# Kernel optimization log

Hardware: AMD Instinct MI355X
Metric: run time of the kernel (lower is better)

Reference implementation:

```python
import jax, jax.numpy as jnp
import numpy as np

C = 128          # channel_size
H = 2            # num_head
HD = C // H      # per-head dim = 64
SCALE = C ** 0.5 # note: module scales by sqrt(channel_size), not sqrt(head_dim)


def setup_inputs() -> dict:
    key = jax.random.key(0)
    k_x, k_w, k_b = jax.random.split(key, 3)
    x = jax.random.normal(k_x, (8, 64, 256, C), dtype=jnp.float32)
    # nn.Linear(C, 3C): weight [3C, C], bias [3C]; y = x @ W.T + b
    bound = 1.0 / np.sqrt(C)
    W_qkv = jax.random.uniform(k_w, (3 * C, C), dtype=jnp.float32, minval=-bound, maxval=bound)
    b_qkv = jax.random.uniform(k_b, (3 * C,), dtype=jnp.float32, minval=-bound, maxval=bound)
    return {"x": x, "W_qkv": W_qkv, "b_qkv": b_qkv}


def reference(x, W_qkv, b_qkv):
    b, l, g, _ = x.shape
    qkv = jnp.einsum('blgc,dc->blgd', x, W_qkv) + b_qkv        # [b,l,g,3C]
    # rearrange 'b l g (d h c) -> d b l h g c'
    qkv = qkv.reshape(b, l, g, 3, H, HD)
    qkv = jnp.transpose(qkv, (3, 0, 1, 4, 2, 5))               # [3,b,l,h,g,c]
    q, k, v = qkv[0], qkv[1], qkv[2]
    score = jnp.einsum('blhgc,blhkc->blhgk', q, k) / SCALE      # [b,l,h,g,g]
    score = jax.nn.softmax(score, axis=-1)
    out = jnp.einsum('blhgk,blhkc->blhgc', score, v)            # [b,l,h,g,c]
    # rearrange 'b l h g c -> b l g (h c)'
    out = jnp.transpose(out, (0, 1, 3, 2, 4)).reshape(b, l, g, H * HD)
    return out
```

## Files before the change

### kernel.cpp

```cpp
#include <hip/hip_runtime.h>
#include <hip/hip_bf16.h>


typedef __bf16 bf16x8 __attribute__((ext_vector_type(8)));
typedef float  f32x4  __attribute__((ext_vector_type(4)));

#define MFMA16(a, b, c) __builtin_amdgcn_mfma_f32_16x16x32_bf16((a), (b), (c), 0, 0, 0)

namespace dmsa {

constexpr int G  = 256;
constexpr int C  = 128;
constexpr int HD = 64;
constexpr float QSCALE = 1.4426950408889634f * 0.08838834764831845f;

__device__ __forceinline__ unsigned pack2(float a, float b) {
    union { __hip_bfloat162 h; unsigned u; } c;
    c.h = __float22bfloat162_rn(make_float2(a, b));
    return c.u;
}
__device__ __forceinline__ uint2 pack4(float a, float b, float c, float d) {
    uint2 r; r.x = pack2(a, b); r.y = pack2(c, d); return r;
}
__device__ __forceinline__ uint4 pack8(const float* p) {
    uint4 r;
    r.x = pack2(p[0], p[1]); r.y = pack2(p[2], p[3]);
    r.z = pack2(p[4], p[5]); r.w = pack2(p[6], p[7]);
    return r;
}
__device__ __forceinline__ bf16x8 lds8(const ushort* p) { return *(const bf16x8*)p; }
__device__ __forceinline__ bf16x8 ldg8(const ushort* p) { return *(const bf16x8*)p; }

__global__ void convw(const float* __restrict__ W, ushort* __restrict__ wbf) {
    int t = blockIdx.x * 256 + threadIdx.x;
    float tmp[8];
    const float* p = W + (size_t)t * 8;
    *(float4*)tmp       = *(const float4*)p;
    *(float4*)(tmp + 4) = *(const float4*)(p + 4);
    *(uint4*)(wbf + (size_t)t * 8) = pack8(tmp);
}

__global__ __launch_bounds__(256)
void prep(const float* __restrict__ x, const ushort* __restrict__ wbf,
          const float* __restrict__ bias, ushort* __restrict__ qb,
          ushort* __restrict__ kb, ushort* __restrict__ vt)
{
    __shared__ ushort xa[64 * 136];
    __shared__ ushort wb[128 * 136];

    const int tid = threadIdx.x, wv = tid >> 6, lane = tid & 63;
    const int l16 = lane & 15, quad = lane >> 4;
    const int mt = blockIdx.x, bl = mt >> 2, g0 = (mt & 3) * 64;

    const float* xg = x + (size_t)mt * 64 * C;
    #pragma unroll
    for (int i = 0; i < 4; ++i) {
        int e = (tid + 256 * i) * 8, r = e >> 7, c = e & 127;
        float tmp[8];
        *(float4*)tmp       = *(const float4*)(xg + r * C + c);
        *(float4*)(tmp + 4) = *(const float4*)(xg + r * C + c + 4);
        *(uint4*)(xa + r * 136 + c) = pack8(tmp);
    }

    for (int nt = 0; nt < 3; ++nt) {
        __syncthreads();
        const ushort* wg = wbf + (size_t)nt * 128 * C;
        #pragma unroll
        for (int i = 0; i < 8; ++i) {
            int e = (tid + 256 * i) * 8, r = e >> 7, c = e & 127;
            *(uint4*)(wb + r * 136 + c) = *(const uint4*)(wg + r * C + c);
        }
        __syncthreads();

        const f32x4 z4 = {0.f, 0.f, 0.f, 0.f};
        if (nt < 2) {
            f32x4 acc[8];
            #pragma unroll
            for (int m = 0; m < 8; ++m) acc[m] = z4;
            #pragma unroll
            for (int kk = 0; kk < 4; ++kk) {
                bf16x8 b = lds8(xa + (wv * 16 + l16) * 136 + kk * 32 + quad * 8);
                #pragma unroll
                for (int m = 0; m < 8; ++m) {
                    bf16x8 a = lds8(wb + (m * 16 + l16) * 136 + kk * 32 + quad * 8);
                    acc[m] = MFMA16(a, b, acc[m]);
                }
            }
            __syncthreads();

            const float scale = (nt == 0) ? QSCALE : 1.0f;
            #pragma unroll
            for (int m = 0; m < 8; ++m) {
                int ch = m * 16 + quad * 4;
                float4 bs = *(const float4*)(bias + nt * C + ch);
                *(uint2*)(wb + (wv * 16 + l16) * 136 + ch) =
                    pack4((acc[m][0] + bs.x) * scale, (acc[m][1] + bs.y) * scale,
                          (acc[m][2] + bs.z) * scale, (acc[m][3] + bs.w) * scale);
            }
            __syncthreads();

            ushort* dst0 = (nt == 0) ? qb : kb;
            #pragma unroll
            for (int h = 0; h < 2; ++h) {
                ushort* dsth = dst0 + ((size_t)(bl * 2 + h) * G + g0) * HD;
                #pragma unroll
                for (int j = 0; j < 2; ++j) {
                    int f = tid + 256 * j;
                    int tok = f >> 3, cc = (f & 7) * 8;
                    *(uint4*)(dsth + tok * HD + cc) =
                        *(const uint4*)(wb + tok * 136 + h * 64 + cc);
                }
            }
        } else {
            f32x4 acc[4][2];
            #pragma unroll
            for (int m = 0; m < 4; ++m)
                #pragma unroll
                for (int n = 0; n < 2; ++n) acc[m][n] = z4;
            #pragma unroll
            for (int kk = 0; kk < 4; ++kk) {
                bf16x8 a[4], b[2];
                #pragma unroll
                for (int m = 0; m < 4; ++m)
                    a[m] = lds8(xa + (m * 16 + l16) * 136 + kk * 32 + quad * 8);
                #pragma unroll
                for (int n = 0; n < 2; ++n)
                    b[n] = lds8(wb + (wv * 32 + n * 16 + l16) * 136 + kk * 32 + quad * 8);
                #pragma unroll
                for (int m = 0; m < 4; ++m)
                    #pragma unroll
                    for (int n = 0; n < 2; ++n)
                        acc[m][n] = MFMA16(a[m], b[n], acc[m][n]);
            }
            __syncthreads();

            #pragma unroll
            for (int n = 0; n < 2; ++n) {
                int ch = wv * 32 + n * 16 + l16;
                float bv = bias[2 * C + ch];
                #pragma unroll
                for (int m = 0; m < 4; ++m) {
                    int tokb = m * 16 + quad * 4;
                    *(uint2*)(wb + ch * 136 + tokb) =
                        pack4(acc[m][n][0] + bv, acc[m][n][1] + bv,
                              acc[m][n][2] + bv, acc[m][n][3] + bv);
                }
            }
            __syncthreads();

            #pragma unroll
            for (int j = 0; j < 4; ++j) {
                int f = tid + 256 * j;
                int ch = f >> 3, gg = (f & 7) * 8;
                int h = ch >> 6, cp = ch & 63;
                *(uint4*)(vt + ((size_t)(bl * 2 + h) * HD + cp) * G + g0 + gg) =
                    *(const uint4*)(wb + ch * 136 + gg);
            }
        }
    }
}

__global__ __launch_bounds__(256)
void attn(const ushort* __restrict__ qb, const ushort* __restrict__ kb,
          const ushort* __restrict__ vt, float* __restrict__ out)
{
    __shared__ ushort kc[2][64 * 72];
    __shared__ ushort vc[2][64 * 72];
    __shared__ ushort pt[4 * 64 * 40];

    const int tid = threadIdx.x, wv = tid >> 6, lane = tid & 63;
    const int l16 = lane & 15, quad = lane >> 4;
    const int bl = blockIdx.x, h = blockIdx.y;

    const size_t blh = (size_t)(bl * 2 + h);
    const ushort* q = qb + blh * G * HD;
    const ushort* k = kb + blh * G * HD;
    const ushort* v = vt + blh * HD * G;
    ushort* ptw = pt + wv * (64 * 40);

    bf16x8 qf[4][2];
    #pragma unroll
    for (int ni = 0; ni < 4; ++ni)
        #pragma unroll
        for (int kk = 0; kk < 2; ++kk)
            qf[ni][kk] = ldg8(q + (size_t)(wv * 64 + ni * 16 + l16) * HD
                              + kk * 32 + quad * 8);

    uint4 kr[2], vr[2];
    #pragma unroll
    for (int j = 0; j < 2; ++j) {
        int f = tid + 256 * j;
        kr[j] = *(const uint4*)(k + f * 8);
        vr[j] = *(const uint4*)(v + (f >> 3) * G + (f & 7) * 8);
    }
    #pragma unroll
    for (int j = 0; j < 2; ++j) {
        int f = tid + 256 * j, row = f >> 3, cc = (f & 7) * 8;
        *(uint4*)(&kc[0][row * 72 + cc]) = kr[j];
        *(uint4*)(&vc[0][row * 72 + cc]) = vr[j];
    }
    __syncthreads();

    const f32x4 z4 = {0.f, 0.f, 0.f, 0.f};
    float lacc[4] = {0.f, 0.f, 0.f, 0.f};
    f32x4 oacc[4][4];
    #pragma unroll
    for (int mi = 0; mi < 4; ++mi)
        #pragma unroll
        for (int ni = 0; ni < 4; ++ni) oacc[mi][ni] = z4;

    for (int c = 0; c < 4; ++c) {
        const int buf = c & 1;
        if (c < 3) {
            #pragma unroll
            for (int j = 0; j < 2; ++j) {
                int f = tid + 256 * j;
                kr[j] = *(const uint4*)(k + (c + 1) * 64 * HD + f * 8);
                vr[j] = *(const uint4*)(v + (f >> 3) * G + (c + 1) * 64 + (f & 7) * 8);
            }
        }

        #pragma unroll
        for (int sub = 0; sub < 2; ++sub) {
            f32x4 s[2][4];
            #pragma unroll
            for (int mi = 0; mi < 2; ++mi)
                #pragma unroll
                for (int ni = 0; ni < 4; ++ni) s[mi][ni] = z4;

            #pragma unroll
            for (int kk = 0; kk < 2; ++kk) {
                bf16x8 kf[2];
                #pragma unroll
                for (int mi = 0; mi < 2; ++mi)
                    kf[mi] = lds8(&kc[buf][(sub * 32 + mi * 16 + l16) * 72
                                           + kk * 32 + quad * 8]);
                #pragma unroll
                for (int mi = 0; mi < 2; ++mi)
                    #pragma unroll
                    for (int ni = 0; ni < 4; ++ni)
                        s[mi][ni] = MFMA16(kf[mi], qf[ni][kk], s[mi][ni]);
            }

            #pragma unroll
            for (int mi = 0; mi < 2; ++mi)
                #pragma unroll
                for (int ni = 0; ni < 4; ++ni) {
                    #pragma unroll
                    for (int r = 0; r < 4; ++r) {
                        float p = exp2f(s[mi][ni][r]);
                        s[mi][ni][r] = p;
                        lacc[ni] += p;
                    }
                    *(uint2*)(ptw + (ni * 16 + l16) * 40 + mi * 16 + quad * 4) =
                        pack4(s[mi][ni][0], s[mi][ni][1], s[mi][ni][2], s[mi][ni][3]);
                }

            bf16x8 pf[4], vf[4];
            #pragma unroll
            for (int ni = 0; ni < 4; ++ni)
                pf[ni] = lds8(ptw + (ni * 16 + l16) * 40 + quad * 8);
            #pragma unroll
            for (int mi = 0; mi < 4; ++mi)
                vf[mi] = lds8(&vc[buf][(mi * 16 + l16) * 72 + sub * 32 + quad * 8]);
            #pragma unroll
            for (int mi = 0; mi < 4; ++mi)
                #pragma unroll
                for (int ni = 0; ni < 4; ++ni)
                    oacc[mi][ni] = MFMA16(vf[mi], pf[ni], oacc[mi][ni]);
        }

        if (c < 3) {
            #pragma unroll
            for (int j = 0; j < 2; ++j) {
                int f = tid + 256 * j, row = f >> 3, cc = (f & 7) * 8;
                *(uint4*)(&kc[buf ^ 1][row * 72 + cc]) = kr[j];
                *(uint4*)(&vc[buf ^ 1][row * 72 + cc]) = vr[j];
            }
        }
        __syncthreads();
    }

    float* og = out + (size_t)bl * G * C + h * HD;
    #pragma unroll
    for (int ni = 0; ni < 4; ++ni) {
        float l = lacc[ni];
        l += __shfl_xor(l, 16);
        l += __shfl_xor(l, 32);
        float inv = 1.0f / l;
        int g = wv * 64 + ni * 16 + l16;
        #pragma unroll
        for (int mi = 0; mi < 4; ++mi) {
            float4 st;
            st.x = oacc[mi][ni][0] * inv; st.y = oacc[mi][ni][1] * inv;
            st.z = oacc[mi][ni][2] * inv; st.w = oacc[mi][ni][3] * inv;
            *(float4*)(og + (size_t)g * C + mi * 16 + quad * 4) = st;
        }
    }
}

}

extern "C" void kernel_launch(void* const* d_in, const int* in_sizes, int n_in,
                              void* d_out, int out_size, void* d_ws, size_t ws_size,
                              hipStream_t stream) {
    (void)in_sizes; (void)n_in; (void)out_size;

    const size_t SEG = (size_t)1024 * 256 * 64;
    if (ws_size < 3 * SEG * 2) return;

    const float* x    = (const float*)d_in[0];
    const float* W    = (const float*)d_in[1];
    const float* bias = (const float*)d_in[2];
    float* out = (float*)d_out;

    ushort* qb = (ushort*)d_ws;
    ushort* kb = qb + SEG;
    ushort* vt = kb + SEG;
    ushort* wbf = (ushort*)((char*)d_out + ((size_t)16777216 * 4 - 131072));

    dmsa::convw<<<dim3(24), dim3(256), 0, stream>>>(W, wbf);
    dmsa::prep<<<dim3(2048), dim3(256), 0, stream>>>(x, wbf, bias, qb, kb, vt);
    dmsa::attn<<<dim3(512, 2), dim3(256), 0, stream>>>(qb, kb, vt, out);
}
```

Before: 193.2 us.

## Split attention queries across blocks and load K/V fragments directly from global

The attention kernel now launches a third grid dimension so each block handles 128 query rows, with each wave owning 32, instead of 256. The shared-memory staging of K and V with double buffering and block barriers is removed. Each wave instead loads its K and V MFMA fragments straight from global memory, relying on L1/L2 for reuse. Launch bounds request 4 blocks per CU. This cuts shared-memory use and synchronisation and doubles the block count for occupancy, but K/V are read from global once per wave (redundantly across waves and blocks) and global-load latency is no longer hidden by explicit prefetch.

```diff
diff --git a/kernel.cpp b/kernel.cpp
--- a/kernel.cpp
+++ b/kernel.cpp
@@ -160,135 +160,104 @@
     }
 }
 
-__global__ __launch_bounds__(256)
+__global__ __launch_bounds__(256, 4)
 void attn(const ushort* __restrict__ qb, const ushort* __restrict__ kb,
           const ushort* __restrict__ vt, float* __restrict__ out)
 {
-    __shared__ ushort kc[2][64 * 72];
-    __shared__ ushort vc[2][64 * 72];
-    __shared__ ushort pt[4 * 64 * 40];
+    __shared__ ushort pt[4 * 32 * 40];
 
     const int tid = threadIdx.x, wv = tid >> 6, lane = tid & 63;
     const int l16 = lane & 15, quad = lane >> 4;
-    const int bl = blockIdx.x, h = blockIdx.y;
+    const int bl = blockIdx.x, h = blockIdx.y, qh = blockIdx.z;
 
     const size_t blh = (size_t)(bl * 2 + h);
     const ushort* q = qb + blh * G * HD;
     const ushort* k = kb + blh * G * HD;
     const ushort* v = vt + blh * HD * G;
-    ushort* ptw = pt + wv * (64 * 40);
-
-    bf16x8 qf[4][2];
-    #pragma unroll
-    for (int ni = 0; ni < 4; ++ni)
+    ushort* ptw = pt + wv * (32 * 40);
+
+    const int gq0 = qh * 128 + wv * 32;
+
+    bf16x8 qf[2][2];
+    #pragma unroll
+    for (int ni = 0; ni < 2; ++ni)
         #pragma unroll
         for (int kk = 0; kk < 2; ++kk)
-            qf[ni][kk] = ldg8(q + (size_t)(wv * 64 + ni * 16 + l16) * HD
+            qf[ni][kk] = ldg8(q + (size_t)(gq0 + ni * 16 + l16) * HD
                               + kk * 32 + quad * 8);
 
-    uint4 kr[2], vr[2];
-    #pragma unroll
-    for (int j = 0; j < 2; ++j) {
-        int f = tid + 256 * j;
-        kr[j] = *(const uint4*)(k + f * 8);
-        vr[j] = *(const uint4*)(v + (f >> 3) * G + (f & 7) * 8);
-    }
-    #pragma unroll
-    for (int j = 0; j < 2; ++j) {
-        int f = tid + 256 * j, row = f >> 3, cc = (f & 7) * 8;
-        *(uint4*)(&kc[0][row * 72 + cc]) = kr[j];
-        *(uint4*)(&vc[0][row * 72 + cc]) = vr[j];
-    }
-    __syncthreads();
-
     const f32x4 z4 = {0.f, 0.f, 0.f, 0.f};
-    float lacc[4] = {0.f, 0.f, 0.f, 0.f};
-    f32x4 oacc[4][4];
+    float lacc[2] = {0.f, 0.f};
+    f32x4 oacc[4][2];
     #pragma unroll
     for (int mi = 0; mi < 4; ++mi)
         #pragma unroll
-        for (int ni = 0; ni < 4; ++ni) oacc[mi][ni] = z4;
-
-    for (int c = 0; c < 4; ++c) {
-        const int buf = c & 1;
-        if (c < 3) {
-            #pragma unroll
-            for (int j = 0; j < 2; ++j) {
-                int f = tid + 256 * j;
-                kr[j] = *(const uint4*)(k + (c + 1) * 64 * HD + f * 8);
-                vr[j] = *(const uint4*)(v + (f >> 3) * G + (c + 1) * 64 + (f & 7) * 8);
-            }
-        }
-
-        #pragma unroll
-        for (int sub = 0; sub < 2; ++sub) {
-            f32x4 s[2][4];
+        for (int ni = 0; ni < 2; ++ni) oacc[mi][ni] = z4;
+
+    #pragma unroll 2
+    for (int sub = 0; sub < 8; ++sub) {
+        const int g0 = sub * 32;
+
+        bf16x8 kf[2][2];
+        #pragma unroll
+        for (int kk = 0; kk < 2; ++kk)
             #pragma unroll
             for (int mi = 0; mi < 2; ++mi)
-                #pragma unroll
-                for (int ni = 0; ni < 4; ++ni) s[mi][ni] = z4;
-
-            #pragma unroll
-            for (int kk = 0; kk < 2; ++kk) {
-                bf16x8 kf[2];
-                #pragma unroll
-                for (int mi = 0; mi < 2; ++mi)
-                    kf[mi] = lds8(&kc[buf][(sub * 32 + mi * 16 + l16) * 72
-                                           + kk * 32 + quad * 8]);
-                #pragma unroll
-                for (int mi = 0; mi < 2; ++mi)
-                    #pragma unroll
-                    for (int ni = 0; ni < 4; ++ni)
-                        s[mi][ni] = MFMA16(kf[mi], qf[ni][kk], s[mi][ni]);
-            }
-
+                kf[kk][mi] = ldg8(k + (size_t)(g0 + mi * 16 + l16) * HD
+                                  + kk * 32 + quad * 8);
+
+        f32x4 s[2][2];
+        #pragma unroll
+        for (int mi = 0; mi < 2; ++mi)
+            #pragma unroll
+            for (int ni = 0; ni < 2; ++ni) s[mi][ni] = z4;
+
+        #pragma unroll
+        for (int kk = 0; kk < 2; ++kk)
             #pragma unroll
             for (int mi = 0; mi < 2; ++mi)
                 #pragma unroll
-                for (int ni = 0; ni < 4; ++ni) {
-                    #pragma unroll
-                    for (int r = 0; r < 4; ++r) {
-                        float p = exp2f(s[mi][ni][r]);
-                        s[mi][ni][r] = p;
-                        lacc[ni] += p;
-                    }
-                    *(uint2*)(ptw + (ni * 16 + l16) * 40 + mi * 16 + quad * 4) =
-                        pack4(s[mi][ni][0], s[mi][ni][1], s[mi][ni][2], s[mi][ni][3]);
-                }
-
-            bf16x8 pf[4], vf[4];
-            #pragma unroll
-            for (int ni = 0; ni < 4; ++ni)
-                pf[ni] = lds8(ptw + (ni * 16 + l16) * 40 + quad * 8);
-            #pragma unroll
-            for (int mi = 0; mi < 4; ++mi)
-                vf[mi] = lds8(&vc[buf][(mi * 16 + l16) * 72 + sub * 32 + quad * 8]);
-            #pragma unroll
-            for (int mi = 0; mi < 4; ++mi)
-                #pragma unroll
-                for (int ni = 0; ni < 4; ++ni)
-                    oacc[mi][ni] = MFMA16(vf[mi], pf[ni], oacc[mi][ni]);
-        }
-
-        if (c < 3) {
-            #pragma unroll
-            for (int j = 0; j < 2; ++j) {
-                int f = tid + 256 * j, row = f >> 3, cc = (f & 7) * 8;
-                *(uint4*)(&kc[buf ^ 1][row * 72 + cc]) = kr[j];
-                *(uint4*)(&vc[buf ^ 1][row * 72 + cc]) = vr[j];
-            }
-        }
-        __syncthreads();
+                for (int ni = 0; ni < 2; ++ni)
+                    s[mi][ni] = MFMA16(kf[kk][mi], qf[ni][kk], s[mi][ni]);
+
+        bf16x8 vf[4];
+        #pragma unroll
+        for (int mi = 0; mi < 4; ++mi)
+            vf[mi] = ldg8(v + (size_t)(mi * 16 + l16) * G + g0 + quad * 8);
+
+        #pragma unroll
+        for (int mi = 0; mi < 2; ++mi)
+            #pragma unroll
+            for (int ni = 0; ni < 2; ++ni) {
+                #pragma unroll
+                for (int r = 0; r < 4; ++r) {
+                    float p = exp2f(s[mi][ni][r]);
+                    s[mi][ni][r] = p;
+                    lacc[ni] += p;
+                }
+                *(uint2*)(ptw + (ni * 16 + l16) * 40 + mi * 16 + quad * 4) =
+                    pack4(s[mi][ni][0], s[mi][ni][1], s[mi][ni][2], s[mi][ni][3]);
+            }
+
+        bf16x8 pf[2];
+        #pragma unroll
+        for (int ni = 0; ni < 2; ++ni)
+            pf[ni] = lds8(ptw + (ni * 16 + l16) * 40 + quad * 8);
+        #pragma unroll
+        for (int mi = 0; mi < 4; ++mi)
+            #pragma unroll
+            for (int ni = 0; ni < 2; ++ni)
+                oacc[mi][ni] = MFMA16(vf[mi], pf[ni], oacc[mi][ni]);
     }
 
     float* og = out + (size_t)bl * G * C + h * HD;
     #pragma unroll
-    for (int ni = 0; ni < 4; ++ni) {
+    for (int ni = 0; ni < 2; ++ni) {
         float l = lacc[ni];
         l += __shfl_xor(l, 16);
         l += __shfl_xor(l, 32);
         float inv = 1.0f / l;
-        int g = wv * 64 + ni * 16 + l16;
+        int g = gq0 + ni * 16 + l16;
         #pragma unroll
         for (int mi = 0; mi < 4; ++mi) {
             float4 st;
@@ -321,5 +290,5 @@
 
     dmsa::convw<<<dim3(24), dim3(256), 0, stream>>>(W, wbf);
     dmsa::prep<<<dim3(2048), dim3(256), 0, stream>>>(x, wbf, bias, qb, kb, vt);
-    dmsa::attn<<<dim3(512, 2), dim3(256), 0, stream>>>(qb, kb, vt, out);
-}
+    dmsa::attn<<<dim3(512, 2, 2), dim3(256), 0, stream>>>(qb, kb, vt, out);
+}
```

New measurement: 208.6 us. +8.0%, slower.
